# Optimization experiments

Hardware: AMD Instinct MI355X
Metric: run time of the kernel (lower is better)

Reference implementation:

```python
import jax, jax.numpy as jnp
import numpy as np
from jax import lax

FPS_NUM = 512
GROUP_NUM = 32
RADIUS = 0.2
BIG = 1e10


def setup_inputs() -> dict:
    key = jax.random.key(0)
    k1, k2 = jax.random.split(key)
    B, N = 8, 32768
    xyz = jax.random.normal(k1, (B, N, 3), dtype=jnp.float32)
    farthest_init = jax.random.randint(k2, (B,), 0, N, dtype=jnp.int32)
    return {"xyz": xyz, "farthest_init": farthest_init}


def _fps(xyz, farthest_init):
    # xyz: [B, N, 3] -> centroids [B, FPS_NUM] int32
    B, N, _ = xyz.shape
    batch_ix = jnp.arange(B)

    def step(carry, _):
        distance, farthest = carry          # [B,N], [B]
        centroid = xyz[batch_ix, farthest]  # [B,3]
        dist = jnp.sum((xyz - centroid[:, None, :]) ** 2, axis=-1)  # [B,N]
        distance = jnp.minimum(distance, dist)
        new_farthest = jnp.argmax(distance, axis=1).astype(farthest.dtype)
        return (distance, new_farthest), farthest

    init = (jnp.full((B, N), BIG, dtype=xyz.dtype), farthest_init)
    _, centroids_t = lax.scan(step, init, None, length=FPS_NUM)  # [FPS_NUM, B]
    return centroids_t.T  # [B, FPS_NUM]


def _ball_query(xyz, centroids_xyz):
    # xyz [B,N,3], centroids_xyz [B,S,3] -> idx [B,S,GROUP_NUM]
    # Pairwise squared distances: [B, S, N]
    dist = jnp.sum((xyz[:, None, :, :] - centroids_xyz[:, :, None, :]) ** 2, axis=-1)
    dist = jnp.where(dist > RADIUS ** 2, BIG, dist)
    idx = jnp.argsort(dist, axis=-1)[:, :, :GROUP_NUM]
    return idx


def reference(xyz, farthest_init):
    centroids = _fps(xyz, farthest_init)                              # [B, S]
    centroids_xyz = jnp.take_along_axis(xyz, centroids[:, :, None], axis=1)  # [B, S, 3]
    group_idx = _ball_query(xyz, centroids_xyz)                       # [B, S, G]
    # gather grouped points per batch: xyz[b][group_idx[b]] -> [B, S, G, 3]
    grouped_xyz = jax.vmap(lambda pts, ix: pts[ix])(xyz, group_idx)
    relative_xyz = grouped_xyz - centroids_xyz[:, :, None, :]
    combined_points = jnp.concatenate(
        [centroids_xyz[:, :, None, :], relative_xyz], axis=2)         # [B, S, G+1, 3]
    return combined_points, centroids_xyz
```

## Files before the change

### kernel.cpp

```cpp
#include <hip/hip_runtime.h>
#include <stdint.h>

#define NPTS   32768
#define NBATCH 8
#define NFPS   512
#define NGRP   32
#define BIGF   1e10f
#define R2F    0.04f
#define CAP    512
#define QPB    8

#define P      8
#define PPB    (NPTS / P)
#define CHUNKS (PPB / 4)
#define THR    1024
#define SLOTB  32

typedef unsigned long long u64;
typedef unsigned int v4u __attribute__((ext_vector_type(4)));
typedef unsigned int v2u __attribute__((ext_vector_type(2)));

__device__ __forceinline__ u64 shfl_xor_u64(u64 v, int off) {
    unsigned lo = (unsigned)v, hi = (unsigned)(v >> 32);
    lo = __shfl_xor(lo, off, 64);
    hi = __shfl_xor(hi, off, 64);
    return ((u64)hi << 32) | lo;
}

__device__ __forceinline__ bool msg_valid(v4u A, v2u B) {
    return ((A.y >> 31) == 0) && (A.x >= 0xFFFF8000u) && (B.x == A.x);
}

__device__ __forceinline__ void mail_store(u64 addr, v4u A, v2u B) {
    asm volatile(
        "global_store_dwordx4 %0, %2, off sc0 sc1\n\t"
        "global_store_dwordx2 %1, %3, off sc0 sc1"
        :: "v"(addr), "v"(addr + 16), "v"(A), "v"(B) : "memory");
}
__device__ __forceinline__ void mail_load(u64 addr, v4u* A, v2u* B) {
    asm volatile(
        "global_load_dwordx4 %0, %2, off sc0 sc1\n\t"
        "global_load_dwordx2 %1, %3, off sc0 sc1\n\t"
        "s_waitcnt vmcnt(0)"
        : "=v"(*A), "=v"(*B) : "v"(addr), "v"(addr + 16) : "memory");
}

__global__ __launch_bounds__(THR) void fps_kernel(
    const float* __restrict__ xyz,
    const int* __restrict__ finit,
    int* __restrict__ cidx,
    u64 mailAddr)
{
#pragma clang fp contract(off)
    const int gb = blockIdx.x;
    const int b  = gb & 7;
    const int me = gb >> 3;
    const int t  = threadIdx.x;
    const float* __restrict__ base = xyz + (size_t)b * (NPTS * 3);

    __shared__ float4 xs4[CHUNKS], ys4[CHUNKS], zs4[CHUNKS];
    __shared__ u64 redK[16];
    __shared__ int farbox;
    __shared__ float cxbox, cybox, czbox;

    float xr[4], yr[4], zr[4], dist[4];
    {
        const float4* __restrict__ g4 =
            reinterpret_cast<const float4*>(base) + 3 * (me * CHUNKS + t);
        const float4 q0 = g4[0];
        const float4 q1 = g4[1];
        const float4 q2 = g4[2];
        xr[0] = q0.x; yr[0] = q0.y; zr[0] = q0.z;
        xr[1] = q0.w; yr[1] = q1.x; zr[1] = q1.y;
        xr[2] = q1.z; yr[2] = q1.w; zr[2] = q2.x;
        xr[3] = q2.y; yr[3] = q2.z; zr[3] = q2.w;
        xs4[t] = make_float4(xr[0], xr[1], xr[2], xr[3]);
        ys4[t] = make_float4(yr[0], yr[1], yr[2], yr[3]);
        zs4[t] = make_float4(zr[0], zr[1], zr[2], zr[3]);
        dist[0] = BIGF; dist[1] = BIGF; dist[2] = BIGF; dist[3] = BIGF;
    }
#pragma unroll
    for (int k = 0; k < 4; ++k) {
        asm("" : "+v"(xr[k]), "+v"(yr[k]), "+v"(zr[k]));
    }

    int far = finit[b];
    float cx = base[3 * far + 0];
    float cy = base[3 * far + 1];
    float cz = base[3 * far + 2];

    const int wid  = t >> 6;
    const int lane = t & 63;

    for (int it = 0; it < NFPS; ++it) {
        if (me == 0 && t == 0) cidx[b * NFPS + it] = far;
        if (it == NFPS - 1) break;

        float vmax = -1.0f;
        int   amax = 0;
        const int gi = me * PPB + 4 * t;
#pragma unroll
        for (int k = 0; k < 4; ++k) {
            float dx = xr[k] - cx;
            float dy = yr[k] - cy;
            float dz = zr[k] - cz;
            float d  = dx * dx + dy * dy;
            d = d + dz * dz;
            float dk = fminf(dist[k], d);
            dist[k] = dk;
            if (dk > vmax) { vmax = dk; amax = gi + k; }
        }

        u64 key = ((u64)__float_as_uint(vmax) << 32)
                | (unsigned)(0xFFFFFFFFu - (unsigned)amax);
#pragma unroll
        for (int off = 32; off >= 1; off >>= 1) {
            u64 o = shfl_xor_u64(key, off);
            key = (o > key) ? o : key;
        }
        if (lane == 0) redK[wid] = key;
        __syncthreads();

        if (wid == 0) {
            u64 blockKey = redK[0];
#pragma unroll
            for (int w = 1; w < 16; ++w) {
                u64 o = redK[w];
                blockKey = (o > blockKey) ? o : blockKey;
            }
            const int gidx = (int)(0xFFFFFFFFu - (unsigned)(blockKey & 0xFFFFFFFFull));
            const int li   = gidx - me * PPB;
            const float candX = reinterpret_cast<const float*>(xs4)[li];
            const float candY = reinterpret_cast<const float*>(ys4)[li];
            const float candZ = reinterpret_cast<const float*>(zs4)[li];

            const u64 slotRow = mailAddr + (u64)((it * NBATCH + b) * P) * SLOTB;
            if (lane == 0) {
                v4u A; v2u B;
                A.x = (unsigned)(blockKey & 0xFFFFFFFFull);
                A.y = (unsigned)(blockKey >> 32);
                A.z = __float_as_uint(candX);
                A.w = __float_as_uint(candY);
                B.x = A.x;
                B.y = __float_as_uint(candZ);
                mail_store(slotRow + (u64)me * SLOTB, A, B);
            }

            u64   k  = 0;
            float px = candX, py = candY, pz = candZ;
            if (lane < P) {
                if (lane == me) {
                    k = blockKey;
                } else {
                    const u64 a = slotRow + (u64)lane * SLOTB;
                    v4u A; v2u B;
                    for (;;) {
                        mail_load(a, &A, &B);
                        if (msg_valid(A, B)) break;
                    }
                    k  = ((u64)A.y << 32) | A.x;
                    px = __uint_as_float(A.z);
                    py = __uint_as_float(A.w);
                    pz = __uint_as_float(B.y);
                }
            }
#pragma unroll
            for (int off = 4; off >= 1; off >>= 1) {
                const u64   ok = shfl_xor_u64(k, off);
                const float ox = __shfl_xor(px, off, 64);
                const float oy = __shfl_xor(py, off, 64);
                const float oz = __shfl_xor(pz, off, 64);
                if (ok > k) { k = ok; px = ox; py = oy; pz = oz; }
            }
            if (lane == 0) {
                farbox = (int)(0xFFFFFFFFu - (unsigned)(k & 0xFFFFFFFFull));
                cxbox = px; cybox = py; czbox = pz;
            }
        }
        __syncthreads();
        far = farbox;
        cx = cxbox; cy = cybox; cz = czbox;
    }
}

__global__ __launch_bounds__(256) void ballq_kernel(
    const float* __restrict__ xyz,
    const int* __restrict__ cidx,
    float* __restrict__ out0,
    float* __restrict__ out1)
{
#pragma clang fp contract(off)
    const int blk0 = blockIdx.x * QPB;
    const int b    = blk0 >> 9;
    const int t    = threadIdx.x;
    const float* __restrict__ base = xyz + (size_t)b * (NPTS * 3);

    __shared__ u64 list[QPB][CAP];
    __shared__ int scnt[QPB];
    __shared__ u64 mask0[QPB];
    __shared__ int selIdx[QPB][NGRP];

    if (t < QPB) scnt[t] = 0;

    float cxs[QPB], cys[QPB], czs[QPB];
#pragma unroll
    for (int q = 0; q < QPB; ++q) {
        const int ci = cidx[blk0 + q];
        cxs[q] = base[3 * ci + 0];
        cys[q] = base[3 * ci + 1];
        czs[q] = base[3 * ci + 2];
    }
    __syncthreads();

    if (t < 64) {
        const float px = base[3 * t + 0];
        const float py = base[3 * t + 1];
        const float pz = base[3 * t + 2];
#pragma unroll
        for (int q = 0; q < QPB; ++q) {
            float dx = px - cxs[q];
            float dy = py - cys[q];
            float dz = pz - czs[q];
            float d  = dx * dx + dy * dy;
            d = d + dz * dz;
            u64 mk = __ballot(d <= R2F);
            if (t == 0) mask0[q] = mk;
        }
    }

    for (int k = 0; k < NPTS / 256; ++k) {
        const int p = k * 256 + t;
        const float px = base[3 * p + 0];
        const float py = base[3 * p + 1];
        const float pz = base[3 * p + 2];
#pragma unroll
        for (int q = 0; q < QPB; ++q) {
            float dx = px - cxs[q];
            float dy = py - cys[q];
            float dz = pz - czs[q];
            float d  = dx * dx + dy * dy;
            d = d + dz * dz;
            if (d <= R2F) {
                int pos = atomicAdd(&scnt[q], 1);
                if (pos < CAP)
                    list[q][pos] = (((u64)__float_as_uint(d)) << 32)
                                   | (unsigned)p;
            }
        }
    }
    __syncthreads();

    {
        const int lane = t & 63;
        for (int q = t >> 6; q < QPB; q += 4) {
            const int m = min(scnt[q], CAP);
            for (int j = lane; j < m; j += 64) {
                const u64 kj = list[q][j];
                int rank = 0;
                for (int i = 0; i < m; ++i) rank += (list[q][i] < kj) ? 1 : 0;
                if (rank < NGRP) selIdx[q][rank] = (int)(kj & 0xffffffffu);
            }
        }
    }
    __syncthreads();

    for (int s = t; s < 33 * QPB; s += 256) {
        const int q    = s / 33;
        const int slot = s % 33;
        const int sg   = blk0 + q;
        const float cx = cxs[q], cy = cys[q], cz = czs[q];
        const size_t o0 = (size_t)sg * 33 * 3;
        if (slot == 32) {
            out0[o0 + 0] = cx; out0[o0 + 1] = cy; out0[o0 + 2] = cz;
            const size_t o1 = (size_t)sg * 3;
            out1[o1 + 0] = cx; out1[o1 + 1] = cy; out1[o1 + 2] = cz;
        } else {
            const int m = min(scnt[q], CAP);
            const int K = min(m, NGRP);
            int idx;
            if (slot < K) {
                idx = selIdx[q][slot];
            } else {
                u64 zeros = ~mask0[q];
                const int need = slot - K;
                for (int z = 0; z < need; ++z) zeros &= zeros - 1;
                idx = __builtin_ctzll(zeros);
            }
            const float px = base[3 * idx + 0];
            const float py = base[3 * idx + 1];
            const float pz = base[3 * idx + 2];
            out0[o0 + (size_t)(1 + slot) * 3 + 0] = px - cx;
            out0[o0 + (size_t)(1 + slot) * 3 + 1] = py - cy;
            out0[o0 + (size_t)(1 + slot) * 3 + 2] = pz - cz;
        }
    }
}

extern "C" void kernel_launch(void* const* d_in, const int* in_sizes, int n_in,
                              void* d_out, int out_size, void* d_ws, size_t ws_size,
                              hipStream_t stream) {
    const float* xyz   = (const float*)d_in[0];
    const int*   finit = (const int*)d_in[1];
    float* out0 = (float*)d_out;
    float* out1 = out0 + (size_t)NBATCH * NFPS * 33 * 3;

    int* cidx = (int*)d_ws;
    u64  mailAddr = (u64)(uintptr_t)((char*)d_ws
                   + (size_t)NBATCH * NFPS * sizeof(int));

    fps_kernel<<<NBATCH * P, THR, 0, stream>>>(xyz, finit, cidx, mailAddr);
    ballq_kernel<<<(NBATCH * NFPS) / QPB, 256, 0, stream>>>(xyz, cidx, out0, out1);
}
```

Before: 1.243 ms.

## Run FPS with one block per batch instead of cross-block mailbox reduction

Replaces the 8-blocks-per-batch FPS, which synchronised blocks through polled global-memory mailboxes each iteration, with a single 1024-thread block per batch holding 32 points per thread. x and y stay in registers as packed float2 vectors, z lives in LDS, and the block-level argmax uses a wavefront shuffle instead of a serial loop. This removes the global-memory polling latency per iteration. In exchange it does 8x more distance work per block on only 8 CUs, adds a dependent global load of the new centroid each iteration, and raises register pressure.

```diff
diff --git a/kernel.cpp b/kernel.cpp
--- a/kernel.cpp
+++ b/kernel.cpp
@@ -10,15 +10,11 @@
 #define CAP    512
 #define QPB    8
 
-#define P      8
-#define PPB    (NPTS / P)
-#define CHUNKS (PPB / 4)
 #define THR    1024
-#define SLOTB  32
+#define NCH    8
 
 typedef unsigned long long u64;
-typedef unsigned int v4u __attribute__((ext_vector_type(4)));
-typedef unsigned int v2u __attribute__((ext_vector_type(2)));
+typedef float v2f __attribute__((ext_vector_type(2)));
 
 __device__ __forceinline__ u64 shfl_xor_u64(u64 v, int off) {
     unsigned lo = (unsigned)v, hi = (unsigned)(v >> 32);
@@ -27,61 +23,42 @@
     return ((u64)hi << 32) | lo;
 }
 
-__device__ __forceinline__ bool msg_valid(v4u A, v2u B) {
-    return ((A.y >> 31) == 0) && (A.x >= 0xFFFF8000u) && (B.x == A.x);
-}
-
-__device__ __forceinline__ void mail_store(u64 addr, v4u A, v2u B) {
-    asm volatile(
-        "global_store_dwordx4 %0, %2, off sc0 sc1\n\t"
-        "global_store_dwordx2 %1, %3, off sc0 sc1"
-        :: "v"(addr), "v"(addr + 16), "v"(A), "v"(B) : "memory");
-}
-__device__ __forceinline__ void mail_load(u64 addr, v4u* A, v2u* B) {
-    asm volatile(
-        "global_load_dwordx4 %0, %2, off sc0 sc1\n\t"
-        "global_load_dwordx2 %1, %3, off sc0 sc1\n\t"
-        "s_waitcnt vmcnt(0)"
-        : "=v"(*A), "=v"(*B) : "v"(addr), "v"(addr + 16) : "memory");
-}
-
 __global__ __launch_bounds__(THR) void fps_kernel(
     const float* __restrict__ xyz,
     const int* __restrict__ finit,
-    int* __restrict__ cidx,
-    u64 mailAddr)
+    int* __restrict__ cidx)
 {
 #pragma clang fp contract(off)
-    const int gb = blockIdx.x;
-    const int b  = gb & 7;
-    const int me = gb >> 3;
-    const int t  = threadIdx.x;
+    const int b = blockIdx.x;
+    const int t = threadIdx.x;
     const float* __restrict__ base = xyz + (size_t)b * (NPTS * 3);
 
-    __shared__ float4 xs4[CHUNKS], ys4[CHUNKS], zs4[CHUNKS];
+    __shared__ float4 zs4[NPTS / 4];
     __shared__ u64 redK[16];
     __shared__ int farbox;
-    __shared__ float cxbox, cybox, czbox;
-
-    float xr[4], yr[4], zr[4], dist[4];
+
+    v2f xr2[2 * NCH], yr2[2 * NCH], dist2[2 * NCH];
     {
-        const float4* __restrict__ g4 =
-            reinterpret_cast<const float4*>(base) + 3 * (me * CHUNKS + t);
-        const float4 q0 = g4[0];
-        const float4 q1 = g4[1];
-        const float4 q2 = g4[2];
-        xr[0] = q0.x; yr[0] = q0.y; zr[0] = q0.z;
-        xr[1] = q0.w; yr[1] = q1.x; zr[1] = q1.y;
-        xr[2] = q1.z; yr[2] = q1.w; zr[2] = q2.x;
-        xr[3] = q2.y; yr[3] = q2.z; zr[3] = q2.w;
-        xs4[t] = make_float4(xr[0], xr[1], xr[2], xr[3]);
-        ys4[t] = make_float4(yr[0], yr[1], yr[2], yr[3]);
-        zs4[t] = make_float4(zr[0], zr[1], zr[2], zr[3]);
-        dist[0] = BIGF; dist[1] = BIGF; dist[2] = BIGF; dist[3] = BIGF;
-    }
-#pragma unroll
-    for (int k = 0; k < 4; ++k) {
-        asm("" : "+v"(xr[k]), "+v"(yr[k]), "+v"(zr[k]));
+        const float4* __restrict__ g4 = reinterpret_cast<const float4*>(base);
+#pragma unroll
+        for (int j = 0; j < NCH; ++j) {
+            const int c = j * THR + t;
+            const float4 q0 = g4[3 * c + 0];
+            const float4 q1 = g4[3 * c + 1];
+            const float4 q2 = g4[3 * c + 2];
+            v2f a;
+            a.x = q0.x; a.y = q0.w;  xr2[2 * j]     = a;
+            a.x = q1.z; a.y = q2.y;  xr2[2 * j + 1] = a;
+            a.x = q0.y; a.y = q1.x;  yr2[2 * j]     = a;
+            a.x = q1.w; a.y = q2.z;  yr2[2 * j + 1] = a;
+            zs4[c] = make_float4(q0.z, q1.y, q2.x, q2.w);
+            a.x = BIGF; a.y = BIGF;
+            dist2[2 * j] = a; dist2[2 * j + 1] = a;
+        }
+    }
+#pragma unroll
+    for (int i = 0; i < 2 * NCH; ++i) {
+        asm("" : "+v"(xr2[i]), "+v"(yr2[i]));
     }
 
     int far = finit[b];
@@ -91,28 +68,53 @@
 
     const int wid  = t >> 6;
     const int lane = t & 63;
+    __syncthreads();
 
     for (int it = 0; it < NFPS; ++it) {
-        if (me == 0 && t == 0) cidx[b * NFPS + it] = far;
+        if (t == 0) cidx[b * NFPS + it] = far;
         if (it == NFPS - 1) break;
 
         float vmax = -1.0f;
         int   amax = 0;
-        const int gi = me * PPB + 4 * t;
-#pragma unroll
-        for (int k = 0; k < 4; ++k) {
-            float dx = xr[k] - cx;
-            float dy = yr[k] - cy;
-            float dz = zr[k] - cz;
-            float d  = dx * dx + dy * dy;
-            d = d + dz * dz;
-            float dk = fminf(dist[k], d);
-            dist[k] = dk;
-            if (dk > vmax) { vmax = dk; amax = gi + k; }
-        }
-
+#pragma unroll
+        for (int j = 0; j < NCH; ++j) {
+            const float4 zq = zs4[j * THR + t];
+            {
+                v2f z; z.x = zq.x; z.y = zq.y;
+                v2f dx = xr2[2 * j] - cx;
+                v2f dy = yr2[2 * j] - cy;
+                v2f dz = z - cz;
+                v2f s0 = dx * dx;
+                v2f s1 = dy * dy;
+                v2f d  = s0 + s1;
+                v2f s2 = dz * dz;
+                d = d + s2;
+                float d0 = fminf(dist2[2 * j].x, d.x);
+                float d1 = fminf(dist2[2 * j].y, d.y);
+                dist2[2 * j].x = d0; dist2[2 * j].y = d1;
+                if (d0 > vmax) { vmax = d0; amax = 4 * j + 0; }
+                if (d1 > vmax) { vmax = d1; amax = 4 * j + 1; }
+            }
+            {
+                v2f z; z.x = zq.z; z.y = zq.w;
+                v2f dx = xr2[2 * j + 1] - cx;
+                v2f dy = yr2[2 * j + 1] - cy;
+                v2f dz = z - cz;
+                v2f s0 = dx * dx;
+                v2f s1 = dy * dy;
+                v2f d  = s0 + s1;
+                v2f s2 = dz * dz;
+                d = d + s2;
+                float d0 = fminf(dist2[2 * j + 1].x, d.x);
+                float d1 = fminf(dist2[2 * j + 1].y, d.y);
+                dist2[2 * j + 1].x = d0; dist2[2 * j + 1].y = d1;
+                if (d0 > vmax) { vmax = d0; amax = 4 * j + 2; }
+                if (d1 > vmax) { vmax = d1; amax = 4 * j + 3; }
+            }
+        }
+        const int gi = ((amax >> 2) << 12) + (t << 2) + (amax & 3);
         u64 key = ((u64)__float_as_uint(vmax) << 32)
-                | (unsigned)(0xFFFFFFFFu - (unsigned)amax);
+                | (u64)(0xFFFFFFFFu - (unsigned)gi);
 #pragma unroll
         for (int off = 32; off >= 1; off >>= 1) {
             u64 o = shfl_xor_u64(key, off);
@@ -122,64 +124,20 @@
         __syncthreads();
 
         if (wid == 0) {
-            u64 blockKey = redK[0];
-#pragma unroll
-            for (int w = 1; w < 16; ++w) {
-                u64 o = redK[w];
-                blockKey = (o > blockKey) ? o : blockKey;
-            }
-            const int gidx = (int)(0xFFFFFFFFu - (unsigned)(blockKey & 0xFFFFFFFFull));
-            const int li   = gidx - me * PPB;
-            const float candX = reinterpret_cast<const float*>(xs4)[li];
-            const float candY = reinterpret_cast<const float*>(ys4)[li];
-            const float candZ = reinterpret_cast<const float*>(zs4)[li];
-
-            const u64 slotRow = mailAddr + (u64)((it * NBATCH + b) * P) * SLOTB;
-            if (lane == 0) {
-                v4u A; v2u B;
-                A.x = (unsigned)(blockKey & 0xFFFFFFFFull);
-                A.y = (unsigned)(blockKey >> 32);
-                A.z = __float_as_uint(candX);
-                A.w = __float_as_uint(candY);
-                B.x = A.x;
-                B.y = __float_as_uint(candZ);
-                mail_store(slotRow + (u64)me * SLOTB, A, B);
-            }
-
-            u64   k  = 0;
-            float px = candX, py = candY, pz = candZ;
-            if (lane < P) {
-                if (lane == me) {
-                    k = blockKey;
-                } else {
-                    const u64 a = slotRow + (u64)lane * SLOTB;
-                    v4u A; v2u B;
-                    for (;;) {
-                        mail_load(a, &A, &B);
-                        if (msg_valid(A, B)) break;
-                    }
-                    k  = ((u64)A.y << 32) | A.x;
-                    px = __uint_as_float(A.z);
-                    py = __uint_as_float(A.w);
-                    pz = __uint_as_float(B.y);
-                }
-            }
-#pragma unroll
-            for (int off = 4; off >= 1; off >>= 1) {
-                const u64   ok = shfl_xor_u64(k, off);
-                const float ox = __shfl_xor(px, off, 64);
-                const float oy = __shfl_xor(py, off, 64);
-                const float oz = __shfl_xor(pz, off, 64);
-                if (ok > k) { k = ok; px = ox; py = oy; pz = oz; }
-            }
-            if (lane == 0) {
+            u64 k = redK[lane & 15];
+#pragma unroll
+            for (int off = 8; off >= 1; off >>= 1) {
+                u64 o = shfl_xor_u64(k, off);
+                k = (o > k) ? o : k;
+            }
+            if (lane == 0)
                 farbox = (int)(0xFFFFFFFFu - (unsigned)(k & 0xFFFFFFFFull));
-                cxbox = px; cybox = py; czbox = pz;
-            }
         }
         __syncthreads();
         far = farbox;
-        cx = cxbox; cy = cybox; cz = czbox;
+        cx = base[3 * far + 0];
+        cy = base[3 * far + 1];
+        cz = base[3 * far + 2];
     }
 }
 
@@ -305,9 +263,7 @@
     float* out1 = out0 + (size_t)NBATCH * NFPS * 33 * 3;
 
     int* cidx = (int*)d_ws;
-    u64  mailAddr = (u64)(uintptr_t)((char*)d_ws
-                   + (size_t)NBATCH * NFPS * sizeof(int));
-
-    fps_kernel<<<NBATCH * P, THR, 0, stream>>>(xyz, finit, cidx, mailAddr);
+
+    fps_kernel<<<NBATCH, THR, 0, stream>>>(xyz, finit, cidx);
     ballq_kernel<<<(NBATCH * NFPS) / QPB, 256, 0, stream>>>(xyz, cidx, out0, out1);
 }
```

After: 1.587 ms. 27.7% more time.
